# Performance work log

Measured on AMD Instinct MI355X. Metric: run time of the kernel, lower is better.

Reference implementation:

```python
import jax, jax.numpy as jnp
import numpy as np

N, B, C = 512, 256, 64          # num_nodes, batch, in_dim (= out_dim since out_dim arg is 0)
CK3, CK4 = C // 2, C            # c_k = int(d**(k-L)*in_dim), d=2, S=2, L=4 -> k=3:32, k=4:64
EPS = 1e-5                      # BatchNorm1d eps


def _ring_hop_indices():
    # Ring graph: node i adjacent to i+-1. DFS hop sets (as the torch __find_k_hops computes):
    #   <=S-hop set (S=2, includes self): [i, i-1, i-2, i+1, i+2]
    #   exact-k sets for k=3,4: [i-k, i+k]
    i = np.arange(N)
    idx_S = np.stack([i, (i - 1) % N, (i - 2) % N, (i + 1) % N, (i + 2) % N], axis=1)
    idx_L3 = np.stack([(i - 3) % N, (i + 3) % N], axis=1)
    idx_L4 = np.stack([(i - 4) % N, (i + 4) % N], axis=1)
    return (jnp.asarray(idx_S, jnp.int32), jnp.asarray(idx_L3, jnp.int32), jnp.asarray(idx_L4, jnp.int32))


def setup_inputs() -> dict:
    key = jax.random.key(0)
    ks = jax.random.split(key, 6)
    idx_S, idx_L3, idx_L4 = _ring_hop_indices()
    s = 1.0 / np.sqrt(C)  # xavier-ish scale
    return {
        "features": jax.random.normal(ks[0], (B, N, C), jnp.float32),
        "A": jax.random.uniform(ks[1], (B, N, N), jnp.float32),
        "W_S": jax.random.normal(ks[2], (N, 5, C, C), jnp.float32) * s,
        "W_L3": jax.random.normal(ks[3], (N, 2, C, CK3), jnp.float32) * s,
        "W_L4": jax.random.normal(ks[4], (N, 2, C, CK4), jnp.float32) * s,
        "Wa": jax.random.normal(ks[5], (C + CK3 + CK4, C), jnp.float32) * s,
        "bn_gamma": jnp.ones((C,), jnp.float32),
        "bn_beta": jnp.zeros((C,), jnp.float32),
        "prelu_a": jnp.full((1,), 0.25, jnp.float32),
        "idx_S": idx_S,
        "idx_L3": idx_L3,
        "idx_L4": idx_L4,
    }


def _hop_mix(features, A, idx, W):
    # features: [B,N,C]; idx: [N,M]; W: [N,M,C,Co]
    g = features[:, idx]                                   # [B,N,M,C]  per-node neighbor gather
    a = A[:, jnp.arange(idx.shape[0])[:, None], idx]       # [B,N,M]    adjacency edge weights
    # sum_m a[b,n,m] * (g[b,n,m,:] @ W[n,m,:,:])
    return jnp.einsum('bnm,bnmc,nmcd->bnd', a, g, W)


def reference(features, A, W_S, W_L3, W_L4, Wa, bn_gamma, bn_beta, prelu_a, idx_S, idx_L3, idx_L4):
    H_S = _hop_mix(features, A, idx_S, W_S)                                   # [B,N,C]
    H_L = jnp.concatenate([_hop_mix(features, A, idx_L3, W_L3),
                           _hop_mix(features, A, idx_L4, W_L4)], axis=-1)     # [B,N,CK3+CK4]
    H_a = jnp.concatenate([H_S, H_L], axis=-1)                                # [B,N,C+total_L]
    H = jnp.einsum('bnf,fo->bno', H_a, Wa)                                    # [B,N,C]
    # BatchNorm1d (training mode): stats over (batch, nodes) per channel, biased variance
    mean = H.mean(axis=(0, 1))
    var = H.var(axis=(0, 1))
    Hn = (H - mean) * jax.lax.rsqrt(var + EPS) * bn_gamma + bn_beta
    # PReLU with a single shared learnable slope
    return jnp.where(Hn > 0, Hn, prelu_a * Hn)
```

## Files before the change

### kernel.cpp

```cpp
#include <hip/hip_runtime.h>
#include <hip/hip_bf16.h>

#define NN 512
#define BB 256

typedef unsigned short u16;
typedef unsigned int u32;
typedef __attribute__((ext_vector_type(8))) short bf16x8;
typedef __attribute__((ext_vector_type(4))) float f32x4;
typedef __attribute__((ext_vector_type(4))) u32 u32x4;

__device__ __forceinline__ u16 f2bf(float x){
  u32 u = __builtin_bit_cast(u32, x);
  u32 r = u + 0x7fffu + ((u >> 16) & 1u);
  return (u16)(r >> 16);
}
__device__ __forceinline__ float bf2f(u16 h){
  return __builtin_bit_cast(float, (u32)h << 16);
}
__device__ __forceinline__ u32 cvtpk(float lo, float hi){
  float2 t; t.x = lo; t.y = hi;
  __hip_bfloat162 h = __float22bfloat162_rn(t);
  u32 r;
  __builtin_memcpy(&r, &h, 4);
  return r;
}
__device__ __forceinline__ bf16x8 pack8nc(float4 u, float4 v){
  u32x4 w;
  w[0] = cvtpk(u.x, u.y);
  w[1] = cvtpk(u.z, u.w);
  w[2] = cvtpk(v.x, v.y);
  w[3] = cvtpk(v.z, v.w);
  return __builtin_bit_cast(bf16x8, w);
}

__global__ __launch_bounds__(256) void k_cast(const float* __restrict__ f, u16* __restrict__ fb){
  int i = blockIdx.x * 256 + threadIdx.x;
  const float4* p = (const float4*)f;
  float4 a = p[2*i], b = p[2*i+1];
  uint4 o;
  o.x = cvtpk(a.x, a.y); o.y = cvtpk(a.z, a.w);
  o.z = cvtpk(b.x, b.y); o.w = cvtpk(b.z, b.w);
  ((uint4*)fb)[i] = o;
}

__global__ __launch_bounds__(256) void k_wat(const float* __restrict__ Wa, u16* __restrict__ wat){
  int t = blockIdx.x * 256 + threadIdx.x;
  int o = t / 192, r = t - o * 192;
  int blk = r >> 6, q = r & 63;
  float v = 0.f;
  if (blk == 0) v = Wa[q * 64 + o];
  else if (blk == 1) { if (q < 32) v = Wa[(64 + q) * 64 + o]; }
  else v = Wa[(96 + q) * 64 + o];
  wat[t] = f2bf(v);
}

__global__ __launch_bounds__(512, 4) void k_main(
    const u16* __restrict__ fb, const float* __restrict__ A,
    const float* __restrict__ WS, const float* __restrict__ WL3, const float* __restrict__ WL4,
    const u16* __restrict__ wat,
    const int* __restrict__ idxS, const int* __restrict__ idxL3, const int* __restrict__ idxL4,
    u16* __restrict__ H, float* __restrict__ bn_part)
{
  int bid = blockIdx.x;
  int n = (bid & 7) * 64 + (bid >> 3);
  int tid = threadIdx.x, lane = tid & 63, wv = tid >> 6;
  int l15 = lane & 15, lg = lane >> 4;

  __shared__ u16 wl[9 * 4096];
  __shared__ float bnl[1024];
  __shared__ int nbrl[9];

  if (tid < 9){
    int v;
    if (tid < 5) v = idxS[n * 5 + tid];
    else if (tid < 7) v = idxL3[n * 2 + (tid - 5)];
    else v = idxL4[n * 2 + (tid - 7)];
    nbrl[tid] = v;
  }

  for (int jj = wv; jj < 9; jj += (wv == 0 ? 8 : 16)){
    const float* src; int jb, cstride;
    if (jj < 5)      { src = WS  + ((size_t)n * 5 + jj)       * 4096; jb = 0; cstride = 64; }
    else if (jj < 7) { src = WL3 + ((size_t)n * 2 + (jj - 5)) * 2048; jb = 1; cstride = 32; }
    else             { src = WL4 + ((size_t)n * 2 + (jj - 7)) * 4096; jb = 2; cstride = 64; }
    char* wlj = (char*)wl + jj * 8192;

    bf16x8 bw[4][2];
    #pragma unroll
    for (int ni = 0; ni < 4; ++ni){
      int c = ni * 16 + l15;
      const float* p = src + c * cstride + lg * 8;
      float4 u = *(const float4*)p, v = *(const float4*)(p + 4);
      bw[ni][0] = pack8nc(u, v);
      if (jb != 1){
        float4 u1 = *(const float4*)(p + 32), v1 = *(const float4*)(p + 36);
        bw[ni][1] = pack8nc(u1, v1);
      }
    }
    #pragma unroll
    for (int h = 0; h < 2; ++h){
      f32x4 fa[2][4];
      #pragma unroll
      for (int mi = 0; mi < 2; ++mi)
        #pragma unroll
        for (int ni = 0; ni < 4; ++ni){ fa[mi][ni][0]=0.f; fa[mi][ni][1]=0.f; fa[mi][ni][2]=0.f; fa[mi][ni][3]=0.f; }
      #pragma unroll
      for (int ks = 0; ks < 2; ++ks){
        if (jb == 1 && ks == 1) continue;
        bf16x8 af0 = *(const bf16x8*)(wat + (h * 32 + l15) * 192      + jb * 64 + ks * 32 + lg * 8);
        bf16x8 af1 = *(const bf16x8*)(wat + (h * 32 + 16 + l15) * 192 + jb * 64 + ks * 32 + lg * 8);
        #pragma unroll
        for (int ni = 0; ni < 4; ++ni){
          fa[0][ni] = __builtin_amdgcn_mfma_f32_16x16x32_bf16(af0, bw[ni][ks], fa[0][ni], 0, 0, 0);
          fa[1][ni] = __builtin_amdgcn_mfma_f32_16x16x32_bf16(af1, bw[ni][ks], fa[1][ni], 0, 0, 0);
        }
      }
      #pragma unroll
      for (int mi = 0; mi < 2; ++mi)
        #pragma unroll
        for (int ni = 0; ni < 4; ++ni)
          #pragma unroll
          for (int r = 0; r < 4; ++r){
            int o = h * 32 + mi * 16 + lg * 4 + r;
            int c = ni * 16 + l15;
            *(u16*)(wlj + o * 128 + ((2 * c) ^ ((o & 7) << 4))) = f2bf(fa[mi][ni][r]);
          }
    }
  }
  __syncthreads();

  int rb = wv * 32;
  const size_t XROW = (size_t)NN * 64;
  const u16* Xb = fb + (size_t)(rb + l15) * XROW;

  f32x4 acc[2][4];
  #pragma unroll
  for (int mi = 0; mi < 2; ++mi)
    #pragma unroll
    for (int ni = 0; ni < 4; ++ni){ acc[mi][ni][0]=0.f; acc[mi][ni][1]=0.f; acc[mi][ni][2]=0.f; acc[mi][ni][3]=0.f; }
  f32x4 kz; kz[0]=0.f; kz[1]=0.f; kz[2]=0.f; kz[3]=0.f;

  #pragma unroll 1
  for (int j = 0; j < 9; ++j){
    int nbrj = nbrl[j];
    const char* wlj = (const char*)wl + j * 8192;

    bf16x8 bfr[2][4];
    #pragma unroll
    for (int ks = 0; ks < 2; ++ks)
      #pragma unroll
      for (int ni = 0; ni < 4; ++ni){
        int d = ni * 16 + l15;
        bfr[ks][ni] = *(const bf16x8*)(wlj + d * 128 + ((ks * 64 + lg * 16) ^ ((d & 7) << 4)));
      }

    #pragma unroll
    for (int mi = 0; mi < 2; ++mi){
      const float* Ap = A + (size_t)(rb + mi * 16 + lg * 4) * (NN * NN) + (size_t)n * NN + nbrj;
      float av0 = Ap[0];
      float av1 = Ap[(size_t)NN * NN];
      float av2 = Ap[(size_t)2 * NN * NN];
      float av3 = Ap[(size_t)3 * NN * NN];
      const u16* xp = Xb + (size_t)(mi * 16) * XROW + nbrj * 64 + lg * 8;
      bf16x8 ax0 = *(const bf16x8*)xp;
      bf16x8 ax1 = *(const bf16x8*)(xp + 32);
      f32x4 P[4];
      #pragma unroll
      for (int ni = 0; ni < 4; ++ni){
        P[ni] = __builtin_amdgcn_mfma_f32_16x16x32_bf16(ax0, bfr[0][ni], kz, 0, 0, 0);
        P[ni] = __builtin_amdgcn_mfma_f32_16x16x32_bf16(ax1, bfr[1][ni], P[ni], 0, 0, 0);
      }
      #pragma unroll
      for (int ni = 0; ni < 4; ++ni){
        acc[mi][ni][0] += av0 * P[ni][0];
        acc[mi][ni][1] += av1 * P[ni][1];
        acc[mi][ni][2] += av2 * P[ni][2];
        acc[mi][ni][3] += av3 * P[ni][3];
      }
    }
  }

  #pragma unroll
  for (int mi = 0; mi < 2; ++mi)
    #pragma unroll
    for (int r = 0; r < 4; ++r){
      int bl = rb + mi * 16 + lg * 4 + r;
      u16* Hr = H + (size_t)bl * (NN * 64) + n * 64;
      #pragma unroll
      for (int ni = 0; ni < 4; ++ni)
        Hr[ni * 16 + l15] = f2bf(acc[mi][ni][r]);
    }

  #pragma unroll
  for (int ni = 0; ni < 4; ++ni){
    float s = 0.f, sq = 0.f;
    #pragma unroll
    for (int mi = 0; mi < 2; ++mi)
      #pragma unroll
      for (int r = 0; r < 4; ++r){ float v = acc[mi][ni][r]; s += v; sq += v * v; }
    s  += __shfl_xor(s, 16);  s  += __shfl_xor(s, 32);
    sq += __shfl_xor(sq, 16); sq += __shfl_xor(sq, 32);
    if (lane < 16){
      bnl[wv * 128 + ni * 16 + lane]      = s;
      bnl[wv * 128 + 64 + ni * 16 + lane] = sq;
    }
  }
  __syncthreads();
  if (tid < 128){
    float s = 0.f;
    #pragma unroll
    for (int w = 0; w < 8; ++w) s += bnl[w * 128 + tid];
    bn_part[(size_t)bid * 128 + tid] = s;
  }
}

__global__ __launch_bounds__(1024) void k_reduce(const float* __restrict__ bn, const float* __restrict__ gamma,
    const float* __restrict__ beta, float* __restrict__ ss){
  __shared__ float red[2048];
  int t = threadIdx.x, d = t & 63, part = t >> 6;
  float s = 0.f, sq = 0.f;
  for (int w = part; w < 512; w += 16){
    s  += bn[w * 128 + d];
    sq += bn[w * 128 + 64 + d];
  }
  red[t] = s; red[1024 + t] = sq;
  __syncthreads();
  if (t < 64){
    float S = 0.f, SQ = 0.f;
    #pragma unroll
    for (int p = 0; p < 16; ++p){ S += red[p * 64 + t]; SQ += red[1024 + p * 64 + t]; }
    float mean = S * (1.f / 131072.f);
    float var  = SQ * (1.f / 131072.f) - mean * mean;
    float sc = gamma[t] * rsqrtf(var + 1e-5f);
    ss[t] = sc;
    ss[64 + t] = beta[t] - mean * sc;
  }
}

__global__ __launch_bounds__(256) void k_apply(const u16* __restrict__ H, const float* __restrict__ ss,
    const float* __restrict__ pa, float* __restrict__ out){
  float a = pa[0];
  int i = blockIdx.x * 256 + threadIdx.x;
  uint4 v = ((const uint4*)H)[i];
  int d0 = (i << 3) & 63;
  float4 sc0 = *(const float4*)(ss + d0);
  float4 sc1 = *(const float4*)(ss + d0 + 4);
  float4 sh0 = *(const float4*)(ss + 64 + d0);
  float4 sh1 = *(const float4*)(ss + 68 + d0);
  float4 o0, o1; float y;
  y = bf2f((u16)(v.x & 0xffff)) * sc0.x + sh0.x; o0.x = y > 0.f ? y : a * y;
  y = bf2f((u16)(v.x >> 16))    * sc0.y + sh0.y; o0.y = y > 0.f ? y : a * y;
  y = bf2f((u16)(v.y & 0xffff)) * sc0.z + sh0.z; o0.z = y > 0.f ? y : a * y;
  y = bf2f((u16)(v.y >> 16))    * sc0.w + sh0.w; o0.w = y > 0.f ? y : a * y;
  y = bf2f((u16)(v.z & 0xffff)) * sc1.x + sh1.x; o1.x = y > 0.f ? y : a * y;
  y = bf2f((u16)(v.z >> 16))    * sc1.y + sh1.y; o1.y = y > 0.f ? y : a * y;
  y = bf2f((u16)(v.w & 0xffff)) * sc1.z + sh1.z; o1.z = y > 0.f ? y : a * y;
  y = bf2f((u16)(v.w >> 16))    * sc1.w + sh1.w; o1.w = y > 0.f ? y : a * y;
  ((float4*)out)[2 * i]     = o0;
  ((float4*)out)[2 * i + 1] = o1;
}

extern "C" void kernel_launch(void* const* d_in, const int* in_sizes, int n_in,
                              void* d_out, int out_size, void* d_ws, size_t ws_size,
                              hipStream_t stream){
  const float* f     = (const float*)d_in[0];
  const float* A     = (const float*)d_in[1];
  const float* WS    = (const float*)d_in[2];
  const float* WL3   = (const float*)d_in[3];
  const float* WL4   = (const float*)d_in[4];
  const float* Wa    = (const float*)d_in[5];
  const float* gamma = (const float*)d_in[6];
  const float* beta  = (const float*)d_in[7];
  const float* pa    = (const float*)d_in[8];
  const int* idxS    = (const int*)d_in[9];
  const int* idxL3   = (const int*)d_in[10];
  const int* idxL4   = (const int*)d_in[11];

  char* ws = (char*)d_ws;
  u16*   fbb = (u16*)(ws);
  u16*   Hb  = (u16*)(ws + 16777216);
  u16*   wat = (u16*)(ws + 33554432);
  float* bnp = (float*)(ws + 33579008);
  float* sss = (float*)(ws + 33841152);

  k_cast  <<<4096, 256, 0, stream>>>(f, fbb);
  k_wat   <<<48,   256, 0, stream>>>(Wa, wat);
  k_main  <<<512,  512, 0, stream>>>(fbb, A, WS, WL3, WL4, wat, idxS, idxL3, idxL4, Hb, bnp);
  k_reduce<<<1,   1024, 0, stream>>>(bnp, gamma, beta, sss);
  k_apply <<<4096, 256, 0, stream>>>(Hb, sss, pa, (float*)d_out);
}
```

Measured before the change: 81.85 us.

## Stage edge weights in LDS and prefetch next neighbor's features

Threads gather all nine adjacency edge weights per batch into LDS as bf16. This gather runs alongside the weight preprocessing, so the inner loop no longer issues strided global loads of A. The main loop now software-prefetches the next neighbor's feature rows and edge weights while the MFMAs for the current neighbor run. The MFMA chain is split per k-step, with each partial scaled into the accumulator. In exchange, A is rounded to bf16, the scaling work per step doubles, the BN scratch reuses the LDS buffer behind an extra barrier, and the extra weight slice moves from wave 0 to wave 7.

```diff
diff --git a/kernel.cpp b/kernel.cpp
--- a/kernel.cpp
+++ b/kernel.cpp
@@ -7,6 +7,7 @@
 typedef unsigned short u16;
 typedef unsigned int u32;
 typedef __attribute__((ext_vector_type(8))) short bf16x8;
+typedef __attribute__((ext_vector_type(4))) short u16x4;
 typedef __attribute__((ext_vector_type(4))) float f32x4;
 typedef __attribute__((ext_vector_type(4))) u32 u32x4;
 
@@ -68,8 +69,8 @@
   int l15 = lane & 15, lg = lane >> 4;
 
   __shared__ u16 wl[9 * 4096];
-  __shared__ float bnl[1024];
-  __shared__ int nbrl[9];
+  __shared__ u16 albf[9 * 256 + 64];
+  __shared__ int nbrl[12];
 
   if (tid < 9){
     int v;
@@ -79,7 +80,20 @@
     nbrl[tid] = v;
   }
 
-  for (int jj = wv; jj < 9; jj += (wv == 0 ? 8 : 16)){
+  if (tid < 256){
+    int b = tid;
+    const float* Ab = A + (size_t)b * (NN * NN) + (size_t)n * NN;
+    #pragma unroll
+    for (int j = 0; j < 9; ++j){
+      int nb;
+      if (j < 5) nb = idxS[n * 5 + j];
+      else if (j < 7) nb = idxL3[n * 2 + (j - 5)];
+      else nb = idxL4[n * 2 + (j - 7)];
+      albf[j * 256 + b] = f2bf(Ab[nb]);
+    }
+  }
+
+  for (int jj = wv; jj < 9; jj += (wv == 7 ? 1 : 16)){
     const float* src; int jb, cstride;
     if (jj < 5)      { src = WS  + ((size_t)n * 5 + jj)       * 4096; jb = 0; cstride = 64; }
     else if (jj < 7) { src = WL3 + ((size_t)n * 2 + (jj - 5)) * 2048; jb = 1; cstride = 32; }
@@ -128,11 +142,19 @@
           }
     }
   }
-  __syncthreads();
 
   int rb = wv * 32;
   const size_t XROW = (size_t)NN * 64;
-  const u16* Xb = fb + (size_t)(rb + l15) * XROW;
+  const u16* xb0 = fb + (size_t)(rb + l15) * XROW + lg * 8;
+  const u16* xb1 = xb0 + (size_t)16 * XROW;
+  int nbr0 = idxS[n * 5];
+  bf16x8 axc[2][2];
+  axc[0][0] = *(const bf16x8*)(xb0 + nbr0 * 64);
+  axc[0][1] = *(const bf16x8*)(xb0 + nbr0 * 64 + 32);
+  axc[1][0] = *(const bf16x8*)(xb1 + nbr0 * 64);
+  axc[1][1] = *(const bf16x8*)(xb1 + nbr0 * 64 + 32);
+
+  __syncthreads();
 
   f32x4 acc[2][4];
   #pragma unroll
@@ -141,42 +163,56 @@
     for (int ni = 0; ni < 4; ++ni){ acc[mi][ni][0]=0.f; acc[mi][ni][1]=0.f; acc[mi][ni][2]=0.f; acc[mi][ni][3]=0.f; }
   f32x4 kz; kz[0]=0.f; kz[1]=0.f; kz[2]=0.f; kz[3]=0.f;
 
+  f32x4 avc[2];
+  #pragma unroll
+  for (int mi = 0; mi < 2; ++mi){
+    u16x4 a4 = *(const u16x4*)(albf + rb + mi * 16 + lg * 4);
+    avc[mi][0] = bf2f((u16)a4[0]); avc[mi][1] = bf2f((u16)a4[1]);
+    avc[mi][2] = bf2f((u16)a4[2]); avc[mi][3] = bf2f((u16)a4[3]);
+  }
+
   #pragma unroll 1
   for (int j = 0; j < 9; ++j){
-    int nbrj = nbrl[j];
+    bf16x8 axn[2][2];
+    f32x4 avn[2];
+    if (j < 8){
+      int nbrn = nbrl[j + 1];
+      axn[0][0] = *(const bf16x8*)(xb0 + nbrn * 64);
+      axn[0][1] = *(const bf16x8*)(xb0 + nbrn * 64 + 32);
+      axn[1][0] = *(const bf16x8*)(xb1 + nbrn * 64);
+      axn[1][1] = *(const bf16x8*)(xb1 + nbrn * 64 + 32);
+      #pragma unroll
+      for (int mi = 0; mi < 2; ++mi){
+        u16x4 a4 = *(const u16x4*)(albf + (j + 1) * 256 + rb + mi * 16 + lg * 4);
+        avn[mi][0] = bf2f((u16)a4[0]); avn[mi][1] = bf2f((u16)a4[1]);
+        avn[mi][2] = bf2f((u16)a4[2]); avn[mi][3] = bf2f((u16)a4[3]);
+      }
+    }
     const char* wlj = (const char*)wl + j * 8192;
-
-    bf16x8 bfr[2][4];
-    #pragma unroll
-    for (int ks = 0; ks < 2; ++ks)
+    #pragma unroll
+    for (int ks = 0; ks < 2; ++ks){
+      bf16x8 bfr[4];
       #pragma unroll
       for (int ni = 0; ni < 4; ++ni){
         int d = ni * 16 + l15;
-        bfr[ks][ni] = *(const bf16x8*)(wlj + d * 128 + ((ks * 64 + lg * 16) ^ ((d & 7) << 4)));
-      }
-
-    #pragma unroll
-    for (int mi = 0; mi < 2; ++mi){
-      const float* Ap = A + (size_t)(rb + mi * 16 + lg * 4) * (NN * NN) + (size_t)n * NN + nbrj;
-      float av0 = Ap[0];
-      float av1 = Ap[(size_t)NN * NN];
-      float av2 = Ap[(size_t)2 * NN * NN];
-      float av3 = Ap[(size_t)3 * NN * NN];
-      const u16* xp = Xb + (size_t)(mi * 16) * XROW + nbrj * 64 + lg * 8;
-      bf16x8 ax0 = *(const bf16x8*)xp;
-      bf16x8 ax1 = *(const bf16x8*)(xp + 32);
-      f32x4 P[4];
-      #pragma unroll
-      for (int ni = 0; ni < 4; ++ni){
-        P[ni] = __builtin_amdgcn_mfma_f32_16x16x32_bf16(ax0, bfr[0][ni], kz, 0, 0, 0);
-        P[ni] = __builtin_amdgcn_mfma_f32_16x16x32_bf16(ax1, bfr[1][ni], P[ni], 0, 0, 0);
-      }
-      #pragma unroll
-      for (int ni = 0; ni < 4; ++ni){
-        acc[mi][ni][0] += av0 * P[ni][0];
-        acc[mi][ni][1] += av1 * P[ni][1];
-        acc[mi][ni][2] += av2 * P[ni][2];
-        acc[mi][ni][3] += av3 * P[ni][3];
+        bfr[ni] = *(const bf16x8*)(wlj + d * 128 + ((ks * 64 + lg * 16) ^ ((d & 7) << 4)));
+      }
+      #pragma unroll
+      for (int mi = 0; mi < 2; ++mi)
+        #pragma unroll
+        for (int ni = 0; ni < 4; ++ni){
+          f32x4 P = __builtin_amdgcn_mfma_f32_16x16x32_bf16(axc[mi][ks], bfr[ni], kz, 0, 0, 0);
+          acc[mi][ni][0] += avc[mi][0] * P[0];
+          acc[mi][ni][1] += avc[mi][1] * P[1];
+          acc[mi][ni][2] += avc[mi][2] * P[2];
+          acc[mi][ni][3] += avc[mi][3] * P[3];
+        }
+    }
+    if (j < 8){
+      #pragma unroll
+      for (int mi = 0; mi < 2; ++mi){
+        axc[mi][0] = axn[mi][0]; axc[mi][1] = axn[mi][1];
+        avc[mi] = avn[mi];
       }
     }
   }
@@ -192,6 +228,8 @@
         Hr[ni * 16 + l15] = f2bf(acc[mi][ni][r]);
     }
 
+  __syncthreads();
+  float* bnl = (float*)albf;
   #pragma unroll
   for (int ni = 0; ni < 4; ++ni){
     float s = 0.f, sq = 0.f;
```

Result: slower. 157.0 us (+91.8%).
